# Performance work log

Measured on AMD Instinct MI355X. Metric: run time of the kernel, lower is better.

## Reference

```python
import jax, jax.numpy as jnp
import numpy as np

ALPHA = 3          # init: alpha
EPS = 1e-6         # init: eps
LOSS_WEIGHT = 1.0  # init: loss_weight
N = 500000


def box2corners(box):
    # (n,5) (x,y,w,h,a) -> (n,4,2) corners, standard differentiable rotated-IoU layout
    x, y, w, h, a = (box[:, i] for i in range(5))
    dx = jnp.array([0.5, -0.5, -0.5, 0.5], box.dtype) * w[:, None]
    dy = jnp.array([0.5, 0.5, -0.5, -0.5], box.dtype) * h[:, None]
    c = jnp.cos(a)[:, None]
    s = jnp.sin(a)[:, None]
    return jnp.stack([dx * c - dy * s + x[:, None], dx * s + dy * c + y[:, None]], -1)


def cross2(a, b):
    return a[..., 0] * b[..., 1] - a[..., 1] * b[..., 0]


def box_intersection(c1, c2):
    # all 4x4 edge-pair segment intersections -> (n,16,2) points, (n,16) validity mask
    p1 = c1[:, :, None, :]                              # (n,4,1,2)
    d1 = jnp.roll(c1, -1, 1)[:, :, None, :] - p1
    q1 = c2[:, None, :, :]                              # (n,1,4,2)
    d2 = jnp.roll(c2, -1, 1)[:, None, :, :] - q1
    den = cross2(d1, d2)
    den_safe = jnp.where(jnp.abs(den) < 1e-12, 1e-12, den)
    t = cross2(q1 - p1, d2) / den_safe
    u = cross2(q1 - p1, d1) / den_safe
    mask = (t > 0) & (t < 1) & (u > 0) & (u < 1)
    pts = (p1 + t[..., None] * d1) * mask[..., None]    # zero invalid, as in torch ref
    n = c1.shape[0]
    return pts.reshape(n, 16, 2), mask.reshape(n, 16)


def corners_in_box(pts, corners):
    # which of pts (n,4,2) lie inside the rotated box given by corners (n,4,2)
    a = corners[:, 0:1]
    b = corners[:, 1:2]
    d = corners[:, 3:4]
    ab = b - a
    ad = d - a
    am = pts - a
    r_ab = jnp.sum(ab * am, -1) / jnp.maximum(jnp.sum(ab * ab, -1), 1e-12)
    r_ad = jnp.sum(ad * am, -1) / jnp.maximum(jnp.sum(ad * ad, -1), 1e-12)
    tol = 1e-6
    return (r_ab > -tol) & (r_ab < 1 + tol) & (r_ad > -tol) & (r_ad < 1 + tol)


def sorted_polygon_area(verts, mask):
    # verts (n,24,2), mask (n,24): sort valid vertices by angle around centroid, shoelace
    mf = mask[..., None].astype(verts.dtype)
    cnt = jnp.maximum(jnp.sum(mf, axis=1, keepdims=True), 1.0)
    center = jnp.sum(verts * mf, axis=1, keepdims=True) / cnt
    rel = verts - center
    ang = jnp.where(mask, jnp.arctan2(rel[..., 1], rel[..., 0]), 1e6)  # invalid -> last
    order = jnp.argsort(ang, axis=1)
    v = jnp.take_along_axis(verts, order[..., None], axis=1)
    ms = jnp.take_along_axis(mask, order, axis=1)
    v = jnp.where(ms[..., None], v, v[:, 0:1, :])  # pad invalid slots with first valid vtx
    nxt = jnp.roll(v, -1, axis=1)
    return 0.5 * jnp.abs(jnp.sum(cross2(v, nxt), axis=1))


def enclosing_smallest(c1, c2):
    # smallest enclosing rotated rectangle over the 8 corners (rotating-calipers over edges)
    pts = jnp.concatenate([c1, c2], axis=1)  # (n,8,2)
    edges = jnp.concatenate([jnp.roll(c1, -1, 1) - c1, jnp.roll(c2, -1, 1) - c2], axis=1)
    u = edges / jnp.maximum(jnp.linalg.norm(edges, axis=-1, keepdims=True), 1e-12)
    perp = jnp.stack([-u[..., 1], u[..., 0]], -1)
    px = jnp.einsum('npc,ndc->npd', pts, u)      # (n,8pts,8dirs)
    py = jnp.einsum('npc,ndc->npd', pts, perp)
    w = px.max(1) - px.min(1)
    h = py.max(1) - py.min(1)
    idx = jnp.argmin(w * h, axis=1)[:, None]
    return jnp.take_along_axis(w, idx, 1)[:, 0], jnp.take_along_axis(h, idx, 1)[:, 0]


def _giou_loss(pred, target):
    c1 = box2corners(pred)
    c2 = box2corners(target)
    inter_pts, inter_mask = box_intersection(c1, c2)
    m1 = corners_in_box(c1, c2)
    m2 = corners_in_box(c2, c1)
    verts = jnp.concatenate([c1, c2, inter_pts], axis=1)  # (n,24,2)
    mask = jnp.concatenate([m1, m2, inter_mask], axis=1)  # (n,24)
    inter_area = sorted_polygon_area(verts, mask)
    union = pred[:, 2] * pred[:, 3] + target[:, 2] * target[:, 3] - inter_area
    ious = jnp.maximum(inter_area / union, EPS)  # ious.clamp(min=eps)
    w, h = enclosing_smallest(c1, c2)
    area_c = w * h
    giou = ious ** ALPHA - ((area_c - union) / area_c) ** ALPHA
    loss = 1.0 - giou
    return LOSS_WEIGHT * jnp.mean(loss)  # reduction='mean'


def setup_inputs() -> dict:
    key = jax.random.key(0)
    ks = jax.random.split(key, 6)
    xy = jax.random.uniform(ks[0], (N, 2), minval=0.0, maxval=1024.0)
    wh1 = jax.random.uniform(ks[1], (N, 2), minval=8.0, maxval=128.0)
    a1 = jax.random.uniform(ks[2], (N, 1), minval=-1.5, maxval=1.5)
    pred = jnp.concatenate([xy, wh1, a1], axis=1)
    xy2 = xy + jax.random.normal(ks[3], (N, 2)) * 8.0  # jitter so boxes mostly overlap
    wh2 = jax.random.uniform(ks[4], (N, 2), minval=8.0, maxval=128.0)
    a2 = jax.random.uniform(ks[5], (N, 1), minval=-1.5, maxval=1.5)
    target = jnp.concatenate([xy2, wh2, a2], axis=1)
    return {"pred": pred, "target": target}


def reference(pred, target):
    return _giou_loss(pred, target)
```

## Files before the change

kernel.cpp:

```cpp
#include <hip/hip_runtime.h>

__device__ __forceinline__ float frcp(float x){ return __builtin_amdgcn_rcpf(x); }

__device__ __forceinline__ float lb_dt(float x0, float y0,
                                       float idx, float idy,
                                       float lx, float hx, float ly, float hy)
{
    float ta = (lx - x0) * idx, tb = (hx - x0) * idx;
    float tc = (ly - y0) * idy, td = (hy - y0) * idy;
    float t0 = fmaxf(fmaxf(fminf(ta, tb), fminf(tc, td)), 0.f);
    float t1 = fminf(fminf(fmaxf(ta, tb), fmaxf(tc, td)), 1.f);
    return fmaxf(t1 - t0, 0.f);
}

__device__ __forceinline__ float clip_quad(float cbx, float cby,
                                           float ux, float uy, float vx, float vy,
                                           float lx, float hx, float ly, float hy)
{
    float upx = ux + vx, upy = uy + vy;
    float umx = ux - vx, umy = uy - vy;
    float g0x = cbx + upx, g0y = cby + upy;
    float g1x = cbx - umx, g1y = cby - umy;
    float g2x = cbx - upx, g2y = cby - upy;
    float g3x = cbx + umx, g3y = cby + umy;

    float iux = frcp(ux + ux), iuy = frcp(uy + uy);
    float ivx = frcp(vx + vx), ivy = frcp(vy + vy);

    float cu  = fmaf(cbx, uy, -cby * ux);
    float cv  = fmaf(cbx, vy, -cby * vx);
    float cuv = fmaf(ux,  vy, -uy  * vx);

    float s;
    s  = lb_dt(g0x, g0y, -iux, -iuy, lx, hx, ly, hy) * (cuv - cu);
    s += lb_dt(g1x, g1y, -ivx, -ivy, lx, hx, ly, hy) * (cuv - cv);
    s += lb_dt(g2x, g2y,  iux,  iuy, lx, hx, ly, hy) * (cuv + cu);
    s += lb_dt(g3x, g3y,  ivx,  ivy, lx, hx, ly, hy) * (cuv + cv);
    return s;
}

__global__ __launch_bounds__(256) void giou_partial_kernel(
    const float* __restrict__ pred, const float* __restrict__ target,
    float* __restrict__ partial, int n)
{
    int i = blockIdx.x * blockDim.x + threadIdx.x;
    float loss = 0.0f;
    if (i < n) {
        const float p0 = pred[5*i+0], p1 = pred[5*i+1], p2 = pred[5*i+2], p3 = pred[5*i+3], p4 = pred[5*i+4];
        const float q0 = target[5*i+0], q1 = target[5*i+1], q2 = target[5*i+2], q3 = target[5*i+3], q4 = target[5*i+4];

        const float oaX = 0.5f*(p0 - q0), oaY = 0.5f*(p1 - q1);
        const float hw1 = 0.5f*p2, hh1 = 0.5f*p3, hw2 = 0.5f*q2, hh2 = 0.5f*q3;

        const float cs1 = __cosf(p4), sn1 = __sinf(p4);
        const float cs2 = __cosf(q4), sn2 = __sinf(q4);
        const float cD = cs1*cs2 + sn1*sn2;
        const float sD = sn2*cs1 - cs2*sn1;

        const float caX =  oaX*cs1 + oaY*sn1;
        const float caY = -oaX*sn1 + oaY*cs1;
        float S = clip_quad(-caX, -caY,
                            cD*hw2,  sD*hw2, -sD*hh2, cD*hh2,
                            caX - hw1, caX + hw1, caY - hh1, caY + hh1);

        const float caX2 =  oaX*cs2 + oaY*sn2;
        const float caY2 = -oaX*sn2 + oaY*cs2;
        S += clip_quad(caX2, caY2,
                       cD*hw1, -sD*hw1, sD*hh1, cD*hh1,
                       -caX2 - hw2, -caX2 + hw2, -caY2 - hh2, -caY2 + hh2);

        float inter_area = fabsf(S);

        float unionv = p2*p3 + q2*q3 - inter_area;
        float iou = fmaxf(inter_area * frcp(unionv), 1e-6f);

        float acd = fabsf(cD), asd = fabsf(sD);
        float eBx = hw2*acd + hh2*asd, eBy = hw2*asd + hh2*acd;
        float w1 = fmaxf(caX + hw1, -caX + eBx) - fminf(caX - hw1, -caX - eBx);
        float h1 = fmaxf(caY + hh1, -caY + eBy) - fminf(caY - hh1, -caY - eBy);
        float a1 = w1*h1;
        float eAx = hw1*acd + hh1*asd, eAy = hw1*asd + hh1*acd;
        float w2 = fmaxf(caX2 + eAx, -caX2 + hw2) - fminf(caX2 - eAx, -caX2 - hw2);
        float h2 = fmaxf(caY2 + eAy, -caY2 + hh2) - fminf(caY2 - eAy, -caY2 - hh2);
        float a2 = w2*h2;

        float area_c = (a2 < a1) ? a2 : a1;

        float r = (area_c - unionv) * frcp(area_c);
        float giou = iou*iou*iou - r*r*r;
        loss = 1.0f - giou;
    }

    #pragma unroll
    for (int off = 32; off; off >>= 1) loss += __shfl_down(loss, off, 64);
    __shared__ float smem[4];
    int lane = threadIdx.x & 63, wid = threadIdx.x >> 6;
    if (lane == 0) smem[wid] = loss;
    __syncthreads();
    if (threadIdx.x == 0) {
        partial[blockIdx.x] = smem[0] + smem[1] + smem[2] + smem[3];
    }
}

__global__ __launch_bounds__(1024) void reduce_final_kernel(
    const float* __restrict__ partial, int nb, float* __restrict__ out, float invn)
{
    int t = threadIdx.x;
    float s = 0.f;
    for (int i2 = t * 2; i2 < nb; i2 += 2048) {
        if (i2 + 1 < nb) { float2 v = *(const float2*)(partial + i2); s += v.x + v.y; }
        else             { s += partial[i2]; }
    }
    #pragma unroll
    for (int off = 32; off; off >>= 1) s += __shfl_down(s, off, 64);
    __shared__ float smem[16];
    int lane = t & 63, wid = t >> 6;
    if (lane == 0) smem[wid] = s;
    __syncthreads();
    if (t == 0) {
        float tot = 0.f;
        #pragma unroll
        for (int k = 0; k < 16; k++) tot += smem[k];
        out[0] = tot * invn;
    }
}

extern "C" void kernel_launch(void* const* d_in, const int* in_sizes, int n_in,
                              void* d_out, int out_size, void* d_ws, size_t ws_size,
                              hipStream_t stream) {
    const float* pred   = (const float*)d_in[0];
    const float* target = (const float*)d_in[1];
    float* out = (float*)d_out;
    float* partial = (float*)d_ws;
    int n  = in_sizes[0] / 5;
    int nb = (n + 255) / 256;
    giou_partial_kernel<<<nb, 256, 0, stream>>>(pred, target, partial, n);
    reduce_final_kernel<<<1, 1024, 0, stream>>>(partial, nb, out, 1.0f/(float)n);
}
```

Measured before the change: 12.93 us.

## Fuse final reduction into main kernel via packed fixed-point atomic counters

Removes the second reduction kernel launch. Each block converts its partial sum to 24-bit-fraction fixed point and packs it with an arrival count into a 64-bit word, then atomically adds it to a per-group slot. The last block in each group forwards the group total to a global slot, and the last group writes the mean. This trades a kernel launch for a memset plus two levels of atomics, and carries a risk of fixed-point overflow or precision loss in the 48-bit value field.

After: 18.17 us. 40.5% more time.

```diff
diff --git a/kernel.cpp b/kernel.cpp
--- a/kernel.cpp
+++ b/kernel.cpp
@@ -39,9 +39,14 @@
     return s;
 }
 
-__global__ __launch_bounds__(256) void giou_partial_kernel(
+#define GROUP_SHIFT 5
+#define SLOT_STRIDE 16
+#define VAL_MASK ((1ULL << 48) - 1ULL)
+
+__global__ __launch_bounds__(256) void giou_kernel(
     const float* __restrict__ pred, const float* __restrict__ target,
-    float* __restrict__ partial, int n)
+    unsigned long long* __restrict__ slots, float* __restrict__ out,
+    int n, int nb, int ngroups, double dscale)
 {
     int i = blockIdx.x * blockDim.x + threadIdx.x;
     float loss = 0.0f;
@@ -97,31 +102,25 @@
     int lane = threadIdx.x & 63, wid = threadIdx.x >> 6;
     if (lane == 0) smem[wid] = loss;
     __syncthreads();
+
     if (threadIdx.x == 0) {
-        partial[blockIdx.x] = smem[0] + smem[1] + smem[2] + smem[3];
-    }
-}
+        float bsum = smem[0] + smem[1] + smem[2] + smem[3];
+        long long fx = llrint((double)bsum * 16777216.0) + (1LL << 30);
+        unsigned long long pack = (1ULL << 48) | (unsigned long long)fx;
 
-__global__ __launch_bounds__(1024) void reduce_final_kernel(
-    const float* __restrict__ partial, int nb, float* __restrict__ out, float invn)
-{
-    int t = threadIdx.x;
-    float s = 0.f;
-    for (int i2 = t * 2; i2 < nb; i2 += 2048) {
-        if (i2 + 1 < nb) { float2 v = *(const float2*)(partial + i2); s += v.x + v.y; }
-        else             { s += partial[i2]; }
-    }
-    #pragma unroll
-    for (int off = 32; off; off >>= 1) s += __shfl_down(s, off, 64);
-    __shared__ float smem[16];
-    int lane = t & 63, wid = t >> 6;
-    if (lane == 0) smem[wid] = s;
-    __syncthreads();
-    if (t == 0) {
-        float tot = 0.f;
-        #pragma unroll
-        for (int k = 0; k < 16; k++) tot += smem[k];
-        out[0] = tot * invn;
+        int g = blockIdx.x >> GROUP_SHIFT;
+        int gsize = min(1 << GROUP_SHIFT, nb - (g << GROUP_SHIFT));
+        unsigned long long old = atomicAdd(&slots[(size_t)g * SLOT_STRIDE], pack);
+        if ((int)(old >> 48) == gsize - 1) {
+            unsigned long long gtot = (old + pack) & VAL_MASK;
+            unsigned long long rpack = (1ULL << 48) | gtot;
+            unsigned long long rold = atomicAdd(&slots[(size_t)ngroups * SLOT_STRIDE], rpack);
+            if ((int)(rold >> 48) == ngroups - 1) {
+                unsigned long long tot = (rold + rpack) & VAL_MASK;
+                long long sval = (long long)tot - ((long long)nb << 30);
+                out[0] = (float)((double)sval * dscale);
+            }
+        }
     }
 }
 
@@ -131,9 +130,12 @@
     const float* pred   = (const float*)d_in[0];
     const float* target = (const float*)d_in[1];
     float* out = (float*)d_out;
-    float* partial = (float*)d_ws;
+    unsigned long long* slots = (unsigned long long*)d_ws;
     int n  = in_sizes[0] / 5;
     int nb = (n + 255) / 256;
-    giou_partial_kernel<<<nb, 256, 0, stream>>>(pred, target, partial, n);
-    reduce_final_kernel<<<1, 1024, 0, stream>>>(partial, nb, out, 1.0f/(float)n);
+    int ngroups = (nb + (1 << GROUP_SHIFT) - 1) >> GROUP_SHIFT;
+    double dscale = 1.0 / (16777216.0 * (double)n);
+    size_t zbytes = ((size_t)ngroups * SLOT_STRIDE + 1) * 8;
+    hipMemsetAsync(d_ws, 0, zbytes, stream);
+    giou_kernel<<<nb, 256, 0, stream>>>(pred, target, slots, out, n, nb, ngroups, dscale);
 }
```
